# Kernel optimization log

Measured on AMD Instinct MI355X. Metric: run time of the kernel, lower is better.

Reference implementation:

```python
import jax, jax.numpy as jnp
import numpy as np

NUM_CAPSULE = 16
DIM_CAPSULE = 32
ROUTINGS = 3


def setup_inputs() -> dict:
    key = jax.random.key(0)
    k1, k2 = jax.random.split(key)
    B, S, D = 256, 512, 256  # batch, input_num_capsule, input_dim_capsule
    x = jax.random.normal(k1, (B, S, D), dtype=jnp.float32)
    # xavier-normal-ish init for W [input_dim_capsule, num_capsule*dim_capsule]
    O = NUM_CAPSULE * DIM_CAPSULE
    std = float(np.sqrt(2.0 / (D + O)))
    W = jax.random.normal(k2, (D, O), dtype=jnp.float32) * std
    return {"x": x, "W": W}


def _squash(v, axis=-1):
    # NOTE: faithful to source: divides by sqrt(||v||^2 + 1e-7) (unit-norm style)
    s = jnp.sum(v * v, axis=axis, keepdims=True)
    return v / jnp.sqrt(s + 1e-7)


def reference(x, W):
    B, S, D = x.shape
    # u_hat: [B, num_capsule, S, dim_capsule]
    u_hat = jnp.einsum('bsd,do->bso', x, W)
    u_hat = u_hat.reshape(B, S, NUM_CAPSULE, DIM_CAPSULE).transpose(0, 2, 1, 3)
    b = jnp.zeros((B, NUM_CAPSULE, S), dtype=u_hat.dtype)
    outputs = None
    for i in range(ROUTINGS):
        # softmax over the num_capsule axis (source permutes then softmax dim=2)
        c = jax.nn.softmax(b, axis=1)  # [B, nc, S]
        outputs = _squash(jnp.einsum('bns,bnsd->bnd', c, u_hat))  # [B, nc, dc]
        if i < ROUTINGS - 1:
            b = jnp.einsum('bnd,bnsd->bns', outputs, u_hat)
    return outputs.reshape(-1, NUM_CAPSULE * DIM_CAPSULE)
```

## Files before the change

### kernel.cpp

```cpp
#include <hip/hip_runtime.h>


#define S_ 512
#define D_ 256
#define O_ 512

typedef __attribute__((ext_vector_type(8))) short short8;
typedef __attribute__((ext_vector_type(4))) float floatx4;

__device__ __forceinline__ unsigned short f2b(float f) {
  union { float ff; unsigned int i; } v; v.ff = f;
  unsigned int u = v.i;
  return (unsigned short)((u + 0x7FFFu + ((u >> 16) & 1u)) >> 16);
}

__global__ __launch_bounds__(512, 2) void caps_kernel(
    const float* __restrict__ x, const float* __restrict__ W,
    float* __restrict__ out)
{
  __shared__ __align__(16) float ytmp[16 * 260];
  __shared__ __align__(16) unsigned short zb[16 * 264];
  __shared__ __align__(16) float outp[O_];
  __shared__ __align__(16) float cbuf[8 * 256];

  const int tid  = threadIdx.x;
  const int wave = tid >> 6;
  const int lane = tid & 63;
  const int l15  = lane & 15;
  const int l4   = lane >> 4;
  const float* xb = x + (size_t)blockIdx.x * (S_ * D_);

  for (int it = 0; it < 3; ++it) {
    if (it == 0) {
      float a0 = 0.f, a1 = 0.f, a2 = 0.f, a3 = 0.f;
      #pragma unroll 4
      for (int r = 0; r < 64; ++r) {
        const int s = (wave << 6) + r;
        const float4 xv = *(const float4*)(xb + s * D_ + (lane << 2));
        a0 += xv.x; a1 += xv.y; a2 += xv.z; a3 += xv.w;
      }
      *(float4*)(cbuf + (wave << 8) + (lane << 2)) = make_float4(a0, a1, a2, a3);
      __syncthreads();
      if (tid < 256) {
        float v = 0.f;
        #pragma unroll
        for (int w = 0; w < 8; ++w) v += cbuf[(w << 8) + tid];
        v *= 0.0625f;
        #pragma unroll
        for (int n = 0; n < 16; ++n) ytmp[n * 260 + tid] = v;
      }
      __syncthreads();
    } else {
      float acc[16][4];
      #pragma unroll
      for (int n = 0; n < 16; ++n) { acc[n][0]=0.f; acc[n][1]=0.f; acc[n][2]=0.f; acc[n][3]=0.f; }
      float* cw = cbuf + (wave << 8);

      #pragma unroll 1
      for (int t = 0; t < 4; ++t) {
        const int s0 = (wave << 6) + (t << 4);
        floatx4 C = {0.f, 0.f, 0.f, 0.f};
        #pragma unroll
        for (int k = 0; k < 8; ++k) {
          const short8 A = *(const short8*)(zb + l15 * 264 + (k << 5) + (l4 << 3));
          const float* xp = xb + (s0 + l15) * D_ + (k << 5) + (l4 << 3);
          const float4 xv0 = *(const float4*)xp;
          const float4 xv1 = *(const float4*)(xp + 4);
          short8 Bf;
          Bf[0] = (short)f2b(xv0.x); Bf[1] = (short)f2b(xv0.y);
          Bf[2] = (short)f2b(xv0.z); Bf[3] = (short)f2b(xv0.w);
          Bf[4] = (short)f2b(xv1.x); Bf[5] = (short)f2b(xv1.y);
          Bf[6] = (short)f2b(xv1.z); Bf[7] = (short)f2b(xv1.w);
          C = __builtin_amdgcn_mfma_f32_16x16x32_bf16(A, Bf, C, 0, 0, 0);
        }
        float m = fmaxf(fmaxf(C[0], C[1]), fmaxf(C[2], C[3]));
        m = fmaxf(m, __shfl_xor(m, 16, 64));
        m = fmaxf(m, __shfl_xor(m, 32, 64));
        const float e0 = __expf(C[0] - m), e1 = __expf(C[1] - m);
        const float e2 = __expf(C[2] - m), e3 = __expf(C[3] - m);
        float sm = e0 + e1 + e2 + e3;
        sm += __shfl_xor(sm, 16, 64);
        sm += __shfl_xor(sm, 32, 64);
        const float inv = 1.f / sm;
        const int nb = l4 << 2;
        cw[(nb + 0) * 16 + l15] = e0 * inv;
        cw[(nb + 1) * 16 + l15] = e1 * inv;
        cw[(nb + 2) * 16 + l15] = e2 * inv;
        cw[(nb + 3) * 16 + l15] = e3 * inv;
        asm volatile("s_waitcnt lgkmcnt(0)" ::: "memory");
        for (int g = 0; g < 4; ++g) {
          float cc[16][4];
          #pragma unroll
          for (int n = 0; n < 16; ++n) {
            const float4 c4 = *(const float4*)(cw + n * 16 + (g << 2));
            cc[n][0] = c4.x; cc[n][1] = c4.y; cc[n][2] = c4.z; cc[n][3] = c4.w;
          }
          #pragma unroll
          for (int j = 0; j < 4; ++j) {
            const float4 xv = *(const float4*)(xb + (s0 + (g << 2) + j) * D_ + (lane << 2));
            #pragma unroll
            for (int n = 0; n < 16; ++n) {
              acc[n][0] += cc[n][j] * xv.x; acc[n][1] += cc[n][j] * xv.y;
              acc[n][2] += cc[n][j] * xv.z; acc[n][3] += cc[n][j] * xv.w;
            }
          }
        }
      }
      for (int rr = 0; rr < 8; ++rr) {
        if (wave == rr) {
          #pragma unroll
          for (int n = 0; n < 16; ++n) {
            float4* p = (float4*)(ytmp + n * 260 + (lane << 2));
            if (rr == 0) { *p = make_float4(acc[n][0], acc[n][1], acc[n][2], acc[n][3]); }
            else { float4 v = *p; v.x += acc[n][0]; v.y += acc[n][1]; v.z += acc[n][2]; v.w += acc[n][3]; *p = v; }
          }
        }
        __syncthreads();
      }
    }

    {
      const int o = tid;
      const int n = o >> 5;
      float a = 0.f;
      for (int Db = 0; Db < 32; ++Db) {
        const float4 y0 = *(const float4*)(ytmp + n * 260 + (Db << 3));
        const float4 y1 = *(const float4*)(ytmp + n * 260 + (Db << 3) + 4);
        const float* wp = W + (size_t)(Db << 3) * O_ + o;
        a += y0.x * wp[0 * O_]; a += y0.y * wp[1 * O_];
        a += y0.z * wp[2 * O_]; a += y0.w * wp[3 * O_];
        a += y1.x * wp[4 * O_]; a += y1.y * wp[5 * O_];
        a += y1.z * wp[6 * O_]; a += y1.w * wp[7 * O_];
      }
      float ss = a * a;
      #pragma unroll
      for (int off = 1; off < 32; off <<= 1) ss += __shfl_xor(ss, off, 64);
      const float v = a / sqrtf(ss + 1e-7f);
      outp[o] = v;
      if (it == 2) out[(size_t)blockIdx.x * O_ + o] = v;
    }
    __syncthreads();

    if (it < 2) {
      {
        const int obase = lane << 3;
        const int n_ln  = lane >> 2;
        float ov[8];
        #pragma unroll
        for (int j = 0; j < 8; ++j) ov[j] = outp[obase + j];
        for (int r = 0; r < 32; ++r) {
          const int Dd = (wave << 5) + r;
          const float4 w0 = *(const float4*)(W + (size_t)Dd * O_ + obase);
          const float4 w1 = *(const float4*)(W + (size_t)Dd * O_ + obase + 4);
          float a = w0.x * ov[0] + w0.y * ov[1] + w0.z * ov[2] + w0.w * ov[3]
                  + w1.x * ov[4] + w1.y * ov[5] + w1.z * ov[6] + w1.w * ov[7];
          a += __shfl_xor(a, 1, 64);
          a += __shfl_xor(a, 2, 64);
          if ((lane & 3) == 0) zb[n_ln * 264 + Dd] = f2b(a);
        }
      }
      __syncthreads();
    }
  }
}

extern "C" void kernel_launch(void* const* d_in, const int* in_sizes, int n_in,
                              void* d_out, int out_size, void* d_ws, size_t ws_size,
                              hipStream_t stream) {
  const float* x = (const float*)d_in[0];
  const float* W = (const float*)d_in[1];
  float* out = (float*)d_out;
  (void)in_sizes; (void)n_in; (void)out_size; (void)d_ws; (void)ws_size;
  caps_kernel<<<256, 512, 0, stream>>>(x, W, out);
}
```

Baseline: 285.9 us.

## Double block to 1024 threads, use LDS atomics for cross-wave reduction

Each block now runs 16 waves instead of 8. Every wave handles 32 input capsules instead of 64, and the W projection is split across two thread halves whose partial sums are combined through shared memory. The serialized 8-step wave-by-wave accumulation into ytmp is replaced by shared-memory float atomicAdd, with ytmp zeroed between iterations. The inner weighted-sum loop is also restructured to load four x rows up front. The aim is more parallelism per batch element and fewer barriers, at the cost of register pressure (launch_bounds 1024,4 with 64 accumulators) and LDS atomic contention.

```diff
diff --git a/kernel.cpp b/kernel.cpp
--- a/kernel.cpp
+++ b/kernel.cpp
@@ -14,14 +14,14 @@
   return (unsigned short)((u + 0x7FFFu + ((u >> 16) & 1u)) >> 16);
 }
 
-__global__ __launch_bounds__(512, 2) void caps_kernel(
+__global__ __launch_bounds__(1024, 4) void caps_kernel(
     const float* __restrict__ x, const float* __restrict__ W,
     float* __restrict__ out)
 {
   __shared__ __align__(16) float ytmp[16 * 260];
   __shared__ __align__(16) unsigned short zb[16 * 264];
   __shared__ __align__(16) float outp[O_];
-  __shared__ __align__(16) float cbuf[8 * 256];
+  __shared__ __align__(16) float cbuf[16 * 256];
 
   const int tid  = threadIdx.x;
   const int wave = tid >> 6;
@@ -34,8 +34,8 @@
     if (it == 0) {
       float a0 = 0.f, a1 = 0.f, a2 = 0.f, a3 = 0.f;
       #pragma unroll 4
-      for (int r = 0; r < 64; ++r) {
-        const int s = (wave << 6) + r;
+      for (int r = 0; r < 32; ++r) {
+        const int s = (wave << 5) + r;
         const float4 xv = *(const float4*)(xb + s * D_ + (lane << 2));
         a0 += xv.x; a1 += xv.y; a2 += xv.z; a3 += xv.w;
       }
@@ -44,7 +44,7 @@
       if (tid < 256) {
         float v = 0.f;
         #pragma unroll
-        for (int w = 0; w < 8; ++w) v += cbuf[(w << 8) + tid];
+        for (int w = 0; w < 16; ++w) v += cbuf[(w << 8) + tid];
         v *= 0.0625f;
         #pragma unroll
         for (int n = 0; n < 16; ++n) ytmp[n * 260 + tid] = v;
@@ -57,8 +57,8 @@
       float* cw = cbuf + (wave << 8);
 
       #pragma unroll 1
-      for (int t = 0; t < 4; ++t) {
-        const int s0 = (wave << 6) + (t << 4);
+      for (int t = 0; t < 2; ++t) {
+        const int s0 = (wave << 5) + (t << 4);
         floatx4 C = {0.f, 0.f, 0.f, 0.f};
         #pragma unroll
         for (int k = 0; k < 8; ++k) {
@@ -88,42 +88,44 @@
         cw[(nb + 2) * 16 + l15] = e2 * inv;
         cw[(nb + 3) * 16 + l15] = e3 * inv;
         asm volatile("s_waitcnt lgkmcnt(0)" ::: "memory");
+        #pragma unroll 1
         for (int g = 0; g < 4; ++g) {
-          float cc[16][4];
+          const float4 xv0g = *(const float4*)(xb + (s0 + (g << 2) + 0) * D_ + (lane << 2));
+          const float4 xv1g = *(const float4*)(xb + (s0 + (g << 2) + 1) * D_ + (lane << 2));
+          const float4 xv2g = *(const float4*)(xb + (s0 + (g << 2) + 2) * D_ + (lane << 2));
+          const float4 xv3g = *(const float4*)(xb + (s0 + (g << 2) + 3) * D_ + (lane << 2));
           #pragma unroll
           for (int n = 0; n < 16; ++n) {
             const float4 c4 = *(const float4*)(cw + n * 16 + (g << 2));
-            cc[n][0] = c4.x; cc[n][1] = c4.y; cc[n][2] = c4.z; cc[n][3] = c4.w;
-          }
-          #pragma unroll
-          for (int j = 0; j < 4; ++j) {
-            const float4 xv = *(const float4*)(xb + (s0 + (g << 2) + j) * D_ + (lane << 2));
-            #pragma unroll
-            for (int n = 0; n < 16; ++n) {
-              acc[n][0] += cc[n][j] * xv.x; acc[n][1] += cc[n][j] * xv.y;
-              acc[n][2] += cc[n][j] * xv.z; acc[n][3] += cc[n][j] * xv.w;
-            }
+            acc[n][0] += c4.x * xv0g.x; acc[n][1] += c4.x * xv0g.y;
+            acc[n][2] += c4.x * xv0g.z; acc[n][3] += c4.x * xv0g.w;
+            acc[n][0] += c4.y * xv1g.x; acc[n][1] += c4.y * xv1g.y;
+            acc[n][2] += c4.y * xv1g.z; acc[n][3] += c4.y * xv1g.w;
+            acc[n][0] += c4.z * xv2g.x; acc[n][1] += c4.z * xv2g.y;
+            acc[n][2] += c4.z * xv2g.z; acc[n][3] += c4.z * xv2g.w;
+            acc[n][0] += c4.w * xv3g.x; acc[n][1] += c4.w * xv3g.y;
+            acc[n][2] += c4.w * xv3g.z; acc[n][3] += c4.w * xv3g.w;
           }
         }
       }
-      for (int rr = 0; rr < 8; ++rr) {
-        if (wave == rr) {
-          #pragma unroll
-          for (int n = 0; n < 16; ++n) {
-            float4* p = (float4*)(ytmp + n * 260 + (lane << 2));
-            if (rr == 0) { *p = make_float4(acc[n][0], acc[n][1], acc[n][2], acc[n][3]); }
-            else { float4 v = *p; v.x += acc[n][0]; v.y += acc[n][1]; v.z += acc[n][2]; v.w += acc[n][3]; *p = v; }
-          }
-        }
-        __syncthreads();
+      #pragma unroll
+      for (int n = 0; n < 16; ++n) {
+        atomicAdd(&ytmp[n * 260 + (lane << 2) + 0], acc[n][0]);
+        atomicAdd(&ytmp[n * 260 + (lane << 2) + 1], acc[n][1]);
+        atomicAdd(&ytmp[n * 260 + (lane << 2) + 2], acc[n][2]);
+        atomicAdd(&ytmp[n * 260 + (lane << 2) + 3], acc[n][3]);
       }
+      __syncthreads();
     }
 
     {
-      const int o = tid;
+      const int o = tid & 511;
+      const int p = tid >> 9;
       const int n = o >> 5;
       float a = 0.f;
-      for (int Db = 0; Db < 32; ++Db) {
+      #pragma unroll 4
+      for (int i = 0; i < 16; ++i) {
+        const int Db = (p << 4) + i;
         const float4 y0 = *(const float4*)(ytmp + n * 260 + (Db << 3));
         const float4 y1 = *(const float4*)(ytmp + n * 260 + (Db << 3) + 4);
         const float* wp = W + (size_t)(Db << 3) * O_ + o;
@@ -132,12 +134,17 @@
         a += y1.x * wp[4 * O_]; a += y1.y * wp[5 * O_];
         a += y1.z * wp[6 * O_]; a += y1.w * wp[7 * O_];
       }
-      float ss = a * a;
-      #pragma unroll
-      for (int off = 1; off < 32; off <<= 1) ss += __shfl_xor(ss, off, 64);
-      const float v = a / sqrtf(ss + 1e-7f);
-      outp[o] = v;
-      if (it == 2) out[(size_t)blockIdx.x * O_ + o] = v;
+      if (p) cbuf[o] = a;
+      __syncthreads();
+      if (!p) {
+        a += cbuf[o];
+        float ss = a * a;
+        #pragma unroll
+        for (int off = 1; off < 32; off <<= 1) ss += __shfl_xor(ss, off, 64);
+        const float v = a / sqrtf(ss + 1e-7f);
+        outp[o] = v;
+        if (it == 2) out[(size_t)blockIdx.x * O_ + o] = v;
+      }
     }
     __syncthreads();
 
@@ -148,8 +155,8 @@
         float ov[8];
         #pragma unroll
         for (int j = 0; j < 8; ++j) ov[j] = outp[obase + j];
-        for (int r = 0; r < 32; ++r) {
-          const int Dd = (wave << 5) + r;
+        for (int r = 0; r < 16; ++r) {
+          const int Dd = (wave << 4) + r;
           const float4 w0 = *(const float4*)(W + (size_t)Dd * O_ + obase);
           const float4 w1 = *(const float4*)(W + (size_t)Dd * O_ + obase + 4);
           float a = w0.x * ov[0] + w0.y * ov[1] + w0.z * ov[2] + w0.w * ov[3]
@@ -159,6 +166,7 @@
           if ((lane & 3) == 0) zb[n_ln * 264 + Dd] = f2b(a);
         }
       }
+      for (int i = tid; i < 16 * 260; i += 1024) ytmp[i] = 0.f;
       __syncthreads();
     }
   }
@@ -171,5 +179,5 @@
   const float* W = (const float*)d_in[1];
   float* out = (float*)d_out;
   (void)in_sizes; (void)n_in; (void)out_size; (void)d_ws; (void)ws_size;
-  caps_kernel<<<256, 512, 0, stream>>>(x, W, out);
+  caps_kernel<<<256, 1024, 0, stream>>>(x, W, out);
 }
```

Result: slower. 630.5 us (+120.5%).

## Compute routing weighted sum with split-bf16 MFMA instead of scalar FMA

Applied to the files above, without the earlier changes.

Replaces the per-wave scalar FMA accumulation of c·x (16 capsules × 256 dims per wave, followed by serialized cross-wave reduction) with MFMA matrix multiplies. Softmax coefficients are written to shared memory as hi/lo bf16 pairs, and x is transposed into double-buffered shared tiles, also split into hi/lo. Three bf16 MFMAs per tile approximate fp32 precision. This removes the heavy VALU work and the 8-step serialized reduction, at the cost of extra shared memory (which may lower occupancy), a barrier per k-chunk, and re-reading and converting x.

```diff
diff --git a/kernel.cpp b/kernel.cpp
--- a/kernel.cpp
+++ b/kernel.cpp
@@ -13,15 +13,20 @@
   unsigned int u = v.i;
   return (unsigned short)((u + 0x7FFFu + ((u >> 16) & 1u)) >> 16);
 }
+__device__ __forceinline__ float b2f(unsigned short h) {
+  union { unsigned int i; float ff; } v; v.i = ((unsigned int)h) << 16;
+  return v.ff;
+}
 
 __global__ __launch_bounds__(512, 2) void caps_kernel(
     const float* __restrict__ x, const float* __restrict__ W,
     float* __restrict__ out)
 {
+  __shared__ __align__(16) unsigned short xT[2][2][256][40];
+  __shared__ __align__(16) unsigned short cds[2][16][552];
   __shared__ __align__(16) float ytmp[16 * 260];
   __shared__ __align__(16) unsigned short zb[16 * 264];
   __shared__ __align__(16) float outp[O_];
-  __shared__ __align__(16) float cbuf[8 * 256];
 
   const int tid  = threadIdx.x;
   const int wave = tid >> 6;
@@ -39,23 +44,19 @@
         const float4 xv = *(const float4*)(xb + s * D_ + (lane << 2));
         a0 += xv.x; a1 += xv.y; a2 += xv.z; a3 += xv.w;
       }
-      *(float4*)(cbuf + (wave << 8) + (lane << 2)) = make_float4(a0, a1, a2, a3);
+      float* rs = (float*)xT;
+      *(float4*)(rs + (wave << 8) + (lane << 2)) = make_float4(a0, a1, a2, a3);
       __syncthreads();
       if (tid < 256) {
         float v = 0.f;
         #pragma unroll
-        for (int w = 0; w < 8; ++w) v += cbuf[(w << 8) + tid];
+        for (int w = 0; w < 8; ++w) v += rs[(w << 8) + tid];
         v *= 0.0625f;
         #pragma unroll
         for (int n = 0; n < 16; ++n) ytmp[n * 260 + tid] = v;
       }
       __syncthreads();
     } else {
-      float acc[16][4];
-      #pragma unroll
-      for (int n = 0; n < 16; ++n) { acc[n][0]=0.f; acc[n][1]=0.f; acc[n][2]=0.f; acc[n][3]=0.f; }
-      float* cw = cbuf + (wave << 8);
-
       #pragma unroll 1
       for (int t = 0; t < 4; ++t) {
         const int s0 = (wave << 6) + (t << 4);
@@ -83,40 +84,69 @@
         sm += __shfl_xor(sm, 32, 64);
         const float inv = 1.f / sm;
         const int nb = l4 << 2;
-        cw[(nb + 0) * 16 + l15] = e0 * inv;
-        cw[(nb + 1) * 16 + l15] = e1 * inv;
-        cw[(nb + 2) * 16 + l15] = e2 * inv;
-        cw[(nb + 3) * 16 + l15] = e3 * inv;
-        asm volatile("s_waitcnt lgkmcnt(0)" ::: "memory");
-        for (int g = 0; g < 4; ++g) {
-          float cc[16][4];
+        const int sc = s0 + l15;
+        float vs[4] = {e0 * inv, e1 * inv, e2 * inv, e3 * inv};
+        #pragma unroll
+        for (int rg = 0; rg < 4; ++rg) {
+          const float v = vs[rg];
+          const unsigned short ch = f2b(v);
+          const unsigned short cl = f2b(v - b2f(ch));
+          cds[0][nb + rg][sc] = ch;
+          cds[1][nb + rg][sc] = cl;
+        }
+      }
+      __syncthreads();
+
+      floatx4 CA = {0.f, 0.f, 0.f, 0.f};
+      floatx4 CB = {0.f, 0.f, 0.f, 0.f};
+      const int dA = wave << 4;
+      const int dB = (wave + 8) << 4;
+      const int d_st = tid & 255;
+      const int s0l  = (tid >> 8) << 4;
+      #pragma unroll 1
+      for (int kc = 0; kc < 16; ++kc) {
+        const int buf = kc & 1;
+        {
+          const float* xs = xb + (size_t)((kc << 5) + s0l) * D_ + d_st;
+          short8 hv0, hv1, lv0, lv1;
           #pragma unroll
-          for (int n = 0; n < 16; ++n) {
-            const float4 c4 = *(const float4*)(cw + n * 16 + (g << 2));
-            cc[n][0] = c4.x; cc[n][1] = c4.y; cc[n][2] = c4.z; cc[n][3] = c4.w;
+          for (int j = 0; j < 8; ++j) {
+            const float v = xs[j * D_];
+            const unsigned short h = f2b(v);
+            hv0[j] = (short)h; lv0[j] = (short)f2b(v - b2f(h));
           }
           #pragma unroll
-          for (int j = 0; j < 4; ++j) {
-            const float4 xv = *(const float4*)(xb + (s0 + (g << 2) + j) * D_ + (lane << 2));
-            #pragma unroll
-            for (int n = 0; n < 16; ++n) {
-              acc[n][0] += cc[n][j] * xv.x; acc[n][1] += cc[n][j] * xv.y;
-              acc[n][2] += cc[n][j] * xv.z; acc[n][3] += cc[n][j] * xv.w;
-            }
+          for (int j = 0; j < 8; ++j) {
+            const float v = xs[(j + 8) * D_];
+            const unsigned short h = f2b(v);
+            hv1[j] = (short)h; lv1[j] = (short)f2b(v - b2f(h));
           }
-        }
-      }
-      for (int rr = 0; rr < 8; ++rr) {
-        if (wave == rr) {
-          #pragma unroll
-          for (int n = 0; n < 16; ++n) {
-            float4* p = (float4*)(ytmp + n * 260 + (lane << 2));
-            if (rr == 0) { *p = make_float4(acc[n][0], acc[n][1], acc[n][2], acc[n][3]); }
-            else { float4 v = *p; v.x += acc[n][0]; v.y += acc[n][1]; v.z += acc[n][2]; v.w += acc[n][3]; *p = v; }
-          }
+          *(short8*)&xT[buf][0][d_st][s0l]     = hv0;
+          *(short8*)&xT[buf][0][d_st][s0l + 8] = hv1;
+          *(short8*)&xT[buf][1][d_st][s0l]     = lv0;
+          *(short8*)&xT[buf][1][d_st][s0l + 8] = lv1;
         }
         __syncthreads();
-      }
+        const short8 Ah  = *(const short8*)&cds[0][l15][(kc << 5) + (l4 << 3)];
+        const short8 Al  = *(const short8*)&cds[1][l15][(kc << 5) + (l4 << 3)];
+        const short8 BAh = *(const short8*)&xT[buf][0][dA + l15][l4 << 3];
+        const short8 BAl = *(const short8*)&xT[buf][1][dA + l15][l4 << 3];
+        const short8 BBh = *(const short8*)&xT[buf][0][dB + l15][l4 << 3];
+        const short8 BBl = *(const short8*)&xT[buf][1][dB + l15][l4 << 3];
+        CA = __builtin_amdgcn_mfma_f32_16x16x32_bf16(Ah, BAh, CA, 0, 0, 0);
+        CA = __builtin_amdgcn_mfma_f32_16x16x32_bf16(Ah, BAl, CA, 0, 0, 0);
+        CA = __builtin_amdgcn_mfma_f32_16x16x32_bf16(Al, BAh, CA, 0, 0, 0);
+        CB = __builtin_amdgcn_mfma_f32_16x16x32_bf16(Ah, BBh, CB, 0, 0, 0);
+        CB = __builtin_amdgcn_mfma_f32_16x16x32_bf16(Ah, BBl, CB, 0, 0, 0);
+        CB = __builtin_amdgcn_mfma_f32_16x16x32_bf16(Al, BBh, CB, 0, 0, 0);
+      }
+      #pragma unroll
+      for (int rg = 0; rg < 4; ++rg)
+        ytmp[((l4 << 2) + rg) * 260 + dA + l15] = CA[rg];
+      #pragma unroll
+      for (int rg = 0; rg < 4; ++rg)
+        ytmp[((l4 << 2) + rg) * 260 + dB + l15] = CB[rg];
+      __syncthreads();
     }
 
     {
```

After: 291.1 us. Within noise of the previous version (+1.8%).

## Compute routing weighted sum with split-bf16 MFMA and LDS atomic reduction

Applied to the files above, without the earlier changes.

The per-capsule weighted sum of x by the softmax coefficients moves from scalar FMAs onto bf16 MFMA instructions. Coefficients and x are each split into high and low bf16 parts, and three MFMAs per tile keep accuracy close to fp32. The serialized eight-step, barrier-per-wave accumulation into shared memory becomes LDS atomicAdd into a zeroed buffer. The ytmp row stride is padded. The cost is more x loads with a strided scalar pattern plus extra conversion work, and a small precision risk from dropping the low-by-low product.

```diff
diff --git a/kernel.cpp b/kernel.cpp
--- a/kernel.cpp
+++ b/kernel.cpp
@@ -13,15 +13,19 @@
   unsigned int u = v.i;
   return (unsigned short)((u + 0x7FFFu + ((u >> 16) & 1u)) >> 16);
 }
+__device__ __forceinline__ float b2f(unsigned short h) {
+  union { unsigned int i; float ff; } v; v.i = ((unsigned int)h) << 16;
+  return v.ff;
+}
 
 __global__ __launch_bounds__(512, 2) void caps_kernel(
     const float* __restrict__ x, const float* __restrict__ W,
     float* __restrict__ out)
 {
-  __shared__ __align__(16) float ytmp[16 * 260];
+  __shared__ __align__(16) float ytmp[16 * 264];
   __shared__ __align__(16) unsigned short zb[16 * 264];
   __shared__ __align__(16) float outp[O_];
-  __shared__ __align__(16) float cbuf[8 * 256];
+  __shared__ __align__(16) unsigned short cds[2][8][16][40];
 
   const int tid  = threadIdx.x;
   const int wave = tid >> 6;
@@ -39,84 +43,89 @@
         const float4 xv = *(const float4*)(xb + s * D_ + (lane << 2));
         a0 += xv.x; a1 += xv.y; a2 += xv.z; a3 += xv.w;
       }
-      *(float4*)(cbuf + (wave << 8) + (lane << 2)) = make_float4(a0, a1, a2, a3);
+      float* rs = (float*)cds;
+      *(float4*)(rs + (wave << 8) + (lane << 2)) = make_float4(a0, a1, a2, a3);
       __syncthreads();
       if (tid < 256) {
         float v = 0.f;
         #pragma unroll
-        for (int w = 0; w < 8; ++w) v += cbuf[(w << 8) + tid];
+        for (int w = 0; w < 8; ++w) v += rs[(w << 8) + tid];
         v *= 0.0625f;
         #pragma unroll
-        for (int n = 0; n < 16; ++n) ytmp[n * 260 + tid] = v;
+        for (int n = 0; n < 16; ++n) ytmp[n * 264 + tid] = v;
       }
       __syncthreads();
     } else {
-      float acc[16][4];
+      floatx4 acc[16];
       #pragma unroll
-      for (int n = 0; n < 16; ++n) { acc[n][0]=0.f; acc[n][1]=0.f; acc[n][2]=0.f; acc[n][3]=0.f; }
-      float* cw = cbuf + (wave << 8);
+      for (int dt = 0; dt < 16; ++dt) acc[dt] = (floatx4){0.f, 0.f, 0.f, 0.f};
 
       #pragma unroll 1
-      for (int t = 0; t < 4; ++t) {
-        const int s0 = (wave << 6) + (t << 4);
-        floatx4 C = {0.f, 0.f, 0.f, 0.f};
-        #pragma unroll
-        for (int k = 0; k < 8; ++k) {
-          const short8 A = *(const short8*)(zb + l15 * 264 + (k << 5) + (l4 << 3));
-          const float* xp = xb + (s0 + l15) * D_ + (k << 5) + (l4 << 3);
-          const float4 xv0 = *(const float4*)xp;
-          const float4 xv1 = *(const float4*)(xp + 4);
-          short8 Bf;
-          Bf[0] = (short)f2b(xv0.x); Bf[1] = (short)f2b(xv0.y);
-          Bf[2] = (short)f2b(xv0.z); Bf[3] = (short)f2b(xv0.w);
-          Bf[4] = (short)f2b(xv1.x); Bf[5] = (short)f2b(xv1.y);
-          Bf[6] = (short)f2b(xv1.z); Bf[7] = (short)f2b(xv1.w);
-          C = __builtin_amdgcn_mfma_f32_16x16x32_bf16(A, Bf, C, 0, 0, 0);
-        }
-        float m = fmaxf(fmaxf(C[0], C[1]), fmaxf(C[2], C[3]));
-        m = fmaxf(m, __shfl_xor(m, 16, 64));
-        m = fmaxf(m, __shfl_xor(m, 32, 64));
-        const float e0 = __expf(C[0] - m), e1 = __expf(C[1] - m);
-        const float e2 = __expf(C[2] - m), e3 = __expf(C[3] - m);
-        float sm = e0 + e1 + e2 + e3;
-        sm += __shfl_xor(sm, 16, 64);
-        sm += __shfl_xor(sm, 32, 64);
-        const float inv = 1.f / sm;
-        const int nb = l4 << 2;
-        cw[(nb + 0) * 16 + l15] = e0 * inv;
-        cw[(nb + 1) * 16 + l15] = e1 * inv;
-        cw[(nb + 2) * 16 + l15] = e2 * inv;
-        cw[(nb + 3) * 16 + l15] = e3 * inv;
-        asm volatile("s_waitcnt lgkmcnt(0)" ::: "memory");
-        for (int g = 0; g < 4; ++g) {
-          float cc[16][4];
+      for (int p = 0; p < 2; ++p) {
+        const int s0p = (wave << 6) + (p << 5);
+        #pragma unroll 1
+        for (int h = 0; h < 2; ++h) {
+          const int s0 = s0p + (h << 4);
+          floatx4 C = {0.f, 0.f, 0.f, 0.f};
           #pragma unroll
-          for (int n = 0; n < 16; ++n) {
-            const float4 c4 = *(const float4*)(cw + n * 16 + (g << 2));
-            cc[n][0] = c4.x; cc[n][1] = c4.y; cc[n][2] = c4.z; cc[n][3] = c4.w;
+          for (int k = 0; k < 8; ++k) {
+            const short8 A = *(const short8*)(zb + l15 * 264 + (k << 5) + (l4 << 3));
+            const float* xp = xb + (s0 + l15) * D_ + (k << 5) + (l4 << 3);
+            const float4 xv0 = *(const float4*)xp;
+            const float4 xv1 = *(const float4*)(xp + 4);
+            short8 Bf;
+            Bf[0] = (short)f2b(xv0.x); Bf[1] = (short)f2b(xv0.y);
+            Bf[2] = (short)f2b(xv0.z); Bf[3] = (short)f2b(xv0.w);
+            Bf[4] = (short)f2b(xv1.x); Bf[5] = (short)f2b(xv1.y);
+            Bf[6] = (short)f2b(xv1.z); Bf[7] = (short)f2b(xv1.w);
+            C = __builtin_amdgcn_mfma_f32_16x16x32_bf16(A, Bf, C, 0, 0, 0);
           }
+          float m = fmaxf(fmaxf(C[0], C[1]), fmaxf(C[2], C[3]));
+          m = fmaxf(m, __shfl_xor(m, 16, 64));
+          m = fmaxf(m, __shfl_xor(m, 32, 64));
+          const float e0 = __expf(C[0] - m), e1 = __expf(C[1] - m);
+          const float e2 = __expf(C[2] - m), e3 = __expf(C[3] - m);
+          float sm = e0 + e1 + e2 + e3;
+          sm += __shfl_xor(sm, 16, 64);
+          sm += __shfl_xor(sm, 32, 64);
+          const float inv = 1.f / sm;
+          const int nb = l4 << 2;
+          const int sc = (h << 4) + l15;
+          float vs[4] = {e0 * inv, e1 * inv, e2 * inv, e3 * inv};
           #pragma unroll
-          for (int j = 0; j < 4; ++j) {
-            const float4 xv = *(const float4*)(xb + (s0 + (g << 2) + j) * D_ + (lane << 2));
-            #pragma unroll
-            for (int n = 0; n < 16; ++n) {
-              acc[n][0] += cc[n][j] * xv.x; acc[n][1] += cc[n][j] * xv.y;
-              acc[n][2] += cc[n][j] * xv.z; acc[n][3] += cc[n][j] * xv.w;
-            }
+          for (int rg = 0; rg < 4; ++rg) {
+            const float v = vs[rg];
+            const unsigned short ch = f2b(v);
+            const unsigned short cl = f2b(v - b2f(ch));
+            cds[0][wave][nb + rg][sc] = ch;
+            cds[1][wave][nb + rg][sc] = cl;
           }
         }
+        asm volatile("s_waitcnt lgkmcnt(0)" ::: "memory");
+        const short8 Ah = *(const short8*)&cds[0][wave][l15][l4 << 3];
+        const short8 Al = *(const short8*)&cds[1][wave][l15][l4 << 3];
+        #pragma unroll
+        for (int dt = 0; dt < 16; ++dt) {
+          const int d0 = dt << 4;
+          short8 Bh, Bl;
+          #pragma unroll
+          for (int j = 0; j < 8; ++j) {
+            const float v = xb[(size_t)(s0p + (l4 << 3) + j) * D_ + d0 + l15];
+            const unsigned short hh = f2b(v);
+            Bh[j] = (short)hh; Bl[j] = (short)f2b(v - b2f(hh));
+          }
+          acc[dt] = __builtin_amdgcn_mfma_f32_16x16x32_bf16(Ah, Bh, acc[dt], 0, 0, 0);
+          acc[dt] = __builtin_amdgcn_mfma_f32_16x16x32_bf16(Al, Bh, acc[dt], 0, 0, 0);
+          acc[dt] = __builtin_amdgcn_mfma_f32_16x16x32_bf16(Ah, Bl, acc[dt], 0, 0, 0);
+        }
       }
-      for (int rr = 0; rr < 8; ++rr) {
-        if (wave == rr) {
-          #pragma unroll
-          for (int n = 0; n < 16; ++n) {
-            float4* p = (float4*)(ytmp + n * 260 + (lane << 2));
-            if (rr == 0) { *p = make_float4(acc[n][0], acc[n][1], acc[n][2], acc[n][3]); }
-            else { float4 v = *p; v.x += acc[n][0]; v.y += acc[n][1]; v.z += acc[n][2]; v.w += acc[n][3]; *p = v; }
-          }
-        }
-        __syncthreads();
+      #pragma unroll
+      for (int dt = 0; dt < 16; ++dt) {
+        #pragma unroll
+        for (int rg = 0; rg < 4; ++rg)
+          atomicAdd(&ytmp[((l4 << 2) + rg) * 264 + (dt << 4) + l15], acc[dt][rg]);
       }
+      __syncthreads();
     }
 
     {
@@ -124,8 +133,8 @@
       const int n = o >> 5;
       float a = 0.f;
       for (int Db = 0; Db < 32; ++Db) {
-        const float4 y0 = *(const float4*)(ytmp + n * 260 + (Db << 3));
-        const float4 y1 = *(const float4*)(ytmp + n * 260 + (Db << 3) + 4);
+        const float4 y0 = *(const float4*)(ytmp + n * 264 + (Db << 3));
+        const float4 y1 = *(const float4*)(ytmp + n * 264 + (Db << 3) + 4);
         const float* wp = W + (size_t)(Db << 3) * O_ + o;
         a += y0.x * wp[0 * O_]; a += y0.y * wp[1 * O_];
         a += y0.z * wp[2 * O_]; a += y0.w * wp[3 * O_];
@@ -159,6 +168,7 @@
           if ((lane & 3) == 0) zb[n_ln * 264 + Dd] = f2b(a);
         }
       }
+      for (int i = tid; i < 16 * 264; i += 512) ytmp[i] = 0.f;
       __syncthreads();
     }
   }
```

Result: slower. 372.0 us (+30.1%).
